# Kernel optimization log

Measured on AMD Instinct MI355X. Metric: run time of the kernel, lower is better.

The kernel has to match this reference:

```python
import jax, jax.numpy as jnp
import numpy as np

B, S, H = 2, 2048, 2048
NH, NKV, HD = 16, 4, 128
GROUPS = NH // NKV  # 4
ROPE_BASE = 10000.0


def _rope_tables(seq_len, dim):
    inv_freq = 1.0 / (ROPE_BASE ** (jnp.arange(0, dim, 2, dtype=jnp.float32) / dim))
    t = jnp.arange(seq_len, dtype=jnp.float32)
    freqs = jnp.outer(t, inv_freq)            # [S, HD/2]
    emb = jnp.concatenate([freqs, freqs], -1)  # [S, HD]
    return jnp.cos(emb), jnp.sin(emb)


def _rotate_half(x):
    x1, x2 = x[..., : x.shape[-1] // 2], x[..., x.shape[-1] // 2:]
    return jnp.concatenate([-x2, x1], axis=-1)


def setup_inputs() -> dict:
    key = jax.random.key(0)
    ks = jax.random.split(key, 5)
    hidden_states = jax.random.normal(ks[0], (B, S, H), dtype=jnp.float32)
    wq = jax.random.normal(ks[1], (H, NH * HD), dtype=jnp.float32) * 0.02
    wk = jax.random.normal(ks[2], (H, NKV * HD), dtype=jnp.float32) * 0.02
    wv = jax.random.normal(ks[3], (H, NKV * HD), dtype=jnp.float32) * 0.02
    wo = jax.random.normal(ks[4], (NH * HD, H), dtype=jnp.float32) * 0.02
    # additive causal mask [1,1,S,S]
    causal = jnp.tril(jnp.ones((S, S), dtype=bool))
    attention_mask = jnp.where(causal, 0.0, jnp.finfo(jnp.float32).min)[None, None]
    return {"hidden_states": hidden_states, "attention_mask": attention_mask,
            "wq": wq, "wk": wk, "wv": wv, "wo": wo}


def reference(hidden_states, attention_mask, wq, wk, wv, wo):
    b, s, _ = hidden_states.shape
    # projections -> [B, heads, S, HD]
    q = (hidden_states @ wq).reshape(b, s, NH, HD).transpose(0, 2, 1, 3)
    k = (hidden_states @ wk).reshape(b, s, NKV, HD).transpose(0, 2, 1, 3)
    v = (hidden_states @ wv).reshape(b, s, NKV, HD).transpose(0, 2, 1, 3)
    cos, sin = _rope_tables(s, HD)             # [S, HD]
    cos = cos[None, None]; sin = sin[None, None]
    q = q * cos + _rotate_half(q) * sin
    k = k * cos + _rotate_half(k) * sin
    # GQA: repeat kv heads (matches repeat_interleave on dim=1)
    k = jnp.repeat(k, GROUPS, axis=1)
    v = jnp.repeat(v, GROUPS, axis=1)
    scores = jnp.einsum("bhqd,bhkd->bhqk", q, k) / jnp.sqrt(jnp.float32(HD))
    scores = scores + attention_mask
    probs = jax.nn.softmax(scores.astype(jnp.float32), axis=-1).astype(q.dtype)
    attn = jnp.einsum("bhqk,bhkd->bhqd", probs, v)
    attn = attn.transpose(0, 2, 1, 3).reshape(b, s, NH * HD)
    return attn @ wo
```

## Files before the change

### kernel.cpp

```cpp
#include <hip/hip_runtime.h>

typedef unsigned short u16;
typedef unsigned int u32;
typedef __attribute__((ext_vector_type(8))) __bf16 bf16x8;
typedef __attribute__((ext_vector_type(8))) u16 u16x8;
typedef __attribute__((ext_vector_type(4))) float f32x4;

#define B_ 2
#define S_ 2048
#define H_ 2048
#define NH_ 16
#define NKV_ 4
#define HD_ 128
#define L2E 1.4426950408889634f

__device__ __forceinline__ u16 f2bf(float f) {
  return __builtin_bit_cast(u16, static_cast<__bf16>(f));
}
__device__ __forceinline__ float bf2f(u16 v) {
  return __builtin_bit_cast(float, (u32)v << 16);
}
__device__ __forceinline__ void gl2lds16(const void* g, void* l) {
  __builtin_amdgcn_global_load_lds((const __attribute__((address_space(1))) u32*)g,
                                   (__attribute__((address_space(3))) u32*)l, 16, 0, 0);
}
__device__ __forceinline__ f32x4 mfma16(bf16x8 a, bf16x8 b, f32x4 c) {
  return __builtin_amdgcn_mfma_f32_16x16x32_bf16(a, b, c, 0, 0, 0);
}

__global__ __launch_bounds__(256) void cvt_f32_bf16(const float* __restrict__ in,
                                                    u16* __restrict__ out) {
  size_t i = ((size_t)blockIdx.x * 256 + threadIdx.x) * 8;
  const float4* p = (const float4*)(in + i);
  float4 a = p[0], b = p[1];
  u16x8 o;
  o[0] = f2bf(a.x); o[1] = f2bf(a.y); o[2] = f2bf(a.z); o[3] = f2bf(a.w);
  o[4] = f2bf(b.x); o[5] = f2bf(b.y); o[6] = f2bf(b.z); o[7] = f2bf(b.w);
  *(u16x8*)(out + i) = o;
}

__global__ __launch_bounds__(256) void transpose_f32_bf16(const float* __restrict__ in,
                                                          u16* __restrict__ out,
                                                          int R, int C) {
  __shared__ float tl[32][33];
  int bx = blockIdx.x, by = blockIdx.y;
  int tx = threadIdx.x & 31, ty = threadIdx.x >> 5;
#pragma unroll
  for (int i = 0; i < 32; i += 8)
    tl[ty + i][tx] = in[(size_t)(by * 32 + ty + i) * C + bx * 32 + tx];
  __syncthreads();
#pragma unroll
  for (int i = 0; i < 32; i += 8)
    out[(size_t)(bx * 32 + ty + i) * R + by * 32 + tx] = f2bf(tl[tx][ty + i]);
}

__global__ __launch_bounds__(256) void transpose_v(const u16* __restrict__ kvb,
                                                   u16* __restrict__ vt) {
  __shared__ u16 tl[32][33];
  int sx = blockIdx.x, dx = blockIdx.y, b = blockIdx.z;
  int tx = threadIdx.x & 31, ty = threadIdx.x >> 5;
#pragma unroll
  for (int i = 0; i < 32; i += 8)
    tl[ty + i][tx] = kvb[(size_t)(b * S_ + sx * 32 + ty + i) * 1024 + 512 + dx * 32 + tx];
  __syncthreads();
#pragma unroll
  for (int i = 0; i < 32; i += 8)
    vt[(size_t)(b * 512 + dx * 32 + ty + i) * 2048 + sx * 32 + tx] = tl[tx][ty + i];
}

__global__ __launch_bounds__(256) void rope_kernel(u16* __restrict__ buf, int rstride,
                                                   int nhshift, float scale) {
  int idx = blockIdx.x * 256 + threadIdx.x;
  int grp = idx & 7;
  int h = (idx >> 3) & ((1 << nhshift) - 1);
  int tok = idx >> (3 + nhshift);
  int s = tok & (S_ - 1);
  u16* p = buf + (size_t)tok * rstride + (h << 7) + grp * 8;
  u16x8 lo = *(u16x8*)p;
  u16x8 hi = *(u16x8*)(p + 64);
  u16x8 olo, ohi;
#pragma unroll
  for (int j = 0; j < 8; j++) {
    int i = grp * 8 + j;
    float inv = exp2f((float)i * -0.20762050593045702f);
    float ang = (float)s * inv;
    float c = cosf(ang) * scale, sn = sinf(ang) * scale;
    float xl = bf2f(lo[j]), xh = bf2f(hi[j]);
    olo[j] = f2bf(xl * c - xh * sn);
    ohi[j] = f2bf(xh * c + xl * sn);
  }
  *(u16x8*)p = olo;
  *(u16x8*)(p + 64) = ohi;
}

template <int MODE>
__global__ __launch_bounds__(256) void gemm_bt(const u16* __restrict__ A,
                                               const u16* __restrict__ BT,
                                               void* __restrict__ C0,
                                               void* __restrict__ C1,
                                               int M, int N, int K) {
  __shared__ u16 As[2 * 128 * 32];
  __shared__ u16 Bs[2 * 128 * 32];
  const int Mt = M >> 7;
  const int nwg = gridDim.x;
  int wg = (blockIdx.x & 7) * (nwg >> 3) + (blockIdx.x >> 3);
  int tm = wg % Mt, tn = wg / Mt;
  const size_t m0 = (size_t)tm << 7, n0 = (size_t)tn << 7;
  const int tid = threadIdx.x;
  const int w = tid >> 6, lane = tid & 63;
  const int g = lane >> 4, l15 = lane & 15;
  const int wr = w >> 1, wc = w & 1;

  const int r0 = tid >> 2, s0 = tid & 3;
  const int r1 = (tid + 256) >> 2, s1 = (tid + 256) & 3;
  const u16* Ar0 = A + (m0 + r0) * K + s0 * 8;
  const u16* Ar1 = A + (m0 + r1) * K + s1 * 8;
  const u16* Br0 = BT + (n0 + r0) * K + s0 * 8;
  const u16* Br1 = BT + (n0 + r1) * K + s1 * 8;

  const f32x4 Z4 = {0.f, 0.f, 0.f, 0.f};
  f32x4 acc[4][4];
#pragma unroll
  for (int m = 0; m < 4; m++)
#pragma unroll
    for (int n = 0; n < 4; n++) acc[m][n] = Z4;

  gl2lds16(Ar0, &As[w * 512]);
  gl2lds16(Ar1, &As[w * 512 + 2048]);
  gl2lds16(Br0, &Bs[w * 512]);
  gl2lds16(Br1, &Bs[w * 512 + 2048]);

  const int nk = K >> 5;
  int cur = 0;
  for (int t = 0; t < nk; ++t) {
    if (t + 1 < nk) {
      const int k0 = (t + 1) << 5;
      const int nb = (cur ^ 1) << 12;
      gl2lds16(Ar0 + k0, &As[nb + w * 512]);
      gl2lds16(Ar1 + k0, &As[nb + w * 512 + 2048]);
      gl2lds16(Br0 + k0, &Bs[nb + w * 512]);
      gl2lds16(Br1 + k0, &Bs[nb + w * 512 + 2048]);
      asm volatile("s_waitcnt vmcnt(4)" ::: "memory");
    } else {
      asm volatile("s_waitcnt vmcnt(0)" ::: "memory");
    }
    __builtin_amdgcn_sched_barrier(0);
    __builtin_amdgcn_s_barrier();
    __builtin_amdgcn_sched_barrier(0);
    const int cb = cur << 12;
    bf16x8 af[4], bfr[4];
#pragma unroll
    for (int m = 0; m < 4; m++)
      af[m] = *(const bf16x8*)&As[cb + (wr * 64 + m * 16 + l15) * 32 + g * 8];
#pragma unroll
    for (int n = 0; n < 4; n++)
      bfr[n] = *(const bf16x8*)&Bs[cb + (wc * 64 + n * 16 + l15) * 32 + g * 8];
#pragma unroll
    for (int m = 0; m < 4; m++)
#pragma unroll
      for (int n = 0; n < 4; n++) acc[m][n] = mfma16(af[m], bfr[n], acc[m][n]);
    __builtin_amdgcn_sched_barrier(0);
    __builtin_amdgcn_s_barrier();
    __builtin_amdgcn_sched_barrier(0);
    cur ^= 1;
  }

  if (MODE == 2) {
    float* C = (float*)C0;
#pragma unroll
    for (int m = 0; m < 4; m++)
#pragma unroll
      for (int n = 0; n < 4; n++)
#pragma unroll
        for (int r = 0; r < 4; r++) {
          size_t row = m0 + wr * 64 + m * 16 + g * 4 + r;
          size_t col = n0 + wc * 64 + n * 16 + l15;
          C[row * (size_t)N + col] = acc[m][n][r];
        }
  } else {
    u16* C;
    size_t cs, cbase;
    if (n0 < 2048) { C = (u16*)C0; cs = 2048; cbase = n0; }
    else           { C = (u16*)C1; cs = 1024; cbase = n0 - 2048; }
#pragma unroll
    for (int m = 0; m < 4; m++)
#pragma unroll
      for (int n = 0; n < 4; n++)
#pragma unroll
        for (int r = 0; r < 4; r++) {
          size_t row = m0 + wr * 64 + m * 16 + g * 4 + r;
          C[row * cs + cbase + wc * 64 + n * 16 + l15] = f2bf(acc[m][n][r]);
        }
  }
}

__global__ __launch_bounds__(256) void attn_kernel(const u16* __restrict__ Qb,
                                                   const u16* __restrict__ KVb,
                                                   const u16* __restrict__ Vt,
                                                   u16* __restrict__ Ob) {
  __shared__ u16 Ks[2][64 * 128];
  __shared__ u16 Vs[2][128 * 64];
  __shared__ u16 Ps[4][16 * 72];
  const int pair = blockIdx.x, h = blockIdx.y, b = blockIdx.z;
  const int kvh = h >> 2;
  const int tid = threadIdx.x, w = tid >> 6, lane = tid & 63;
  const int g = lane >> 4, l15 = lane & 15;
  const f32x4 Z4 = {0.f, 0.f, 0.f, 0.f};
  u16x8 oneu;
#pragma unroll
  for (int j = 0; j < 8; j++) oneu[j] = 0x3f80;
  const bf16x8 ones = __builtin_bit_cast(bf16x8, oneu);

  const u16* Kbase = KVb + (size_t)b * S_ * 1024 + kvh * 128;
  const u16* Vbase = Vt + (size_t)(b * NKV_ + kvh) * HD_ * 2048;

  for (int half = 0; half < 2; ++half) {
    const int qt = half ? pair : 31 - pair;
    const int qrow0 = qt * 64 + w * 16;

    bf16x8 qf[4];
    const u16* qp = Qb + (size_t)(b * S_ + qrow0 + l15) * 2048 + h * 128;
#pragma unroll
    for (int ds = 0; ds < 4; ds++) qf[ds] = *(const bf16x8*)(qp + ds * 32 + g * 8);

    float m_r[4], l_r[4];
    f32x4 oa[8];
#pragma unroll
    for (int r = 0; r < 4; r++) { m_r[r] = -1e30f; l_r[r] = 0.f; }
#pragma unroll
    for (int n = 0; n < 8; n++) oa[n] = Z4;

    const int nt = qt + 1;
#pragma unroll
    for (int ro = 0; ro < 4; ++ro) {
      int c = ro * 256 + tid;
      int kv = c >> 4, p = c & 15;
      gl2lds16(Kbase + (size_t)kv * 1024 + 8 * (p ^ (kv & 15)), &Ks[0][ro * 2048 + w * 512]);
      int d = c >> 3, p2 = c & 7;
      gl2lds16(Vbase + (size_t)d * 2048 + 8 * (p2 ^ (d & 7)), &Vs[0][ro * 2048 + w * 512]);
    }
    __syncthreads();
    int cur = 0;

    for (int t = 0; t < nt; ++t) {
      const int kv0 = t * 64;
      if (t + 1 < nt) {
        const int nkv0 = kv0 + 64;
#pragma unroll
        for (int ro = 0; ro < 4; ++ro) {
          int c = ro * 256 + tid;
          int kv = c >> 4, p = c & 15;
          gl2lds16(Kbase + (size_t)(nkv0 + kv) * 1024 + 8 * (p ^ (kv & 15)),
                   &Ks[cur ^ 1][ro * 2048 + w * 512]);
          int d = c >> 3, p2 = c & 7;
          gl2lds16(Vbase + (size_t)d * 2048 + nkv0 + 8 * (p2 ^ (d & 7)),
                   &Vs[cur ^ 1][ro * 2048 + w * 512]);
        }
      }

      f32x4 sa[4];
#pragma unroll
      for (int c16 = 0; c16 < 4; c16++) sa[c16] = Z4;
      __builtin_amdgcn_s_setprio(1);
#pragma unroll
      for (int ds = 0; ds < 4; ++ds) {
#pragma unroll
        for (int c16 = 0; c16 < 4; ++c16) {
          bf16x8 kf = *(const bf16x8*)&Ks[cur][(c16 * 16 + l15) * 128 + ((ds * 4 + g) ^ l15) * 8];
          sa[c16] = mfma16(qf[ds], kf, sa[c16]);
        }
      }
      __builtin_amdgcn_s_setprio(0);

      if (kv0 + 63 > qrow0) {
#pragma unroll
        for (int c16 = 0; c16 < 4; c16++)
#pragma unroll
          for (int r = 0; r < 4; r++) {
            if (kv0 + c16 * 16 + l15 > qrow0 + g * 4 + r) sa[c16][r] = -1e30f;
          }
      }

      float lmax[4];
#pragma unroll
      for (int r = 0; r < 4; r++)
        lmax[r] = fmaxf(fmaxf(sa[0][r], sa[1][r]), fmaxf(sa[2][r], sa[3][r]));
      bool need = (lmax[0] > m_r[0] + 8.f) || (lmax[1] > m_r[1] + 8.f) ||
                  (lmax[2] > m_r[2] + 8.f) || (lmax[3] > m_r[3] + 8.f);
      if (__any(need)) {
        float pm[4];
#pragma unroll
        for (int r = 0; r < 4; r++) pm[r] = lmax[r];
#pragma unroll
        for (int off = 1; off < 16; off <<= 1)
#pragma unroll
          for (int r = 0; r < 4; r++) pm[r] = fmaxf(pm[r], __shfl_xor(pm[r], off));
#pragma unroll
        for (int r = 0; r < 4; r++) {
          float mn = fmaxf(m_r[r], pm[r]);
          float corr = exp2f((m_r[r] - mn) * L2E);
          m_r[r] = mn;
          l_r[r] *= corr;
#pragma unroll
          for (int n = 0; n < 8; n++) oa[n][r] *= corr;
        }
      }

#pragma unroll
      for (int c16 = 0; c16 < 4; c16++)
#pragma unroll
        for (int r = 0; r < 4; r++)
          Ps[w][(g * 4 + r) * 72 + c16 * 16 + l15] =
              f2bf(exp2f((sa[c16][r] - m_r[r]) * L2E));
      asm volatile("s_waitcnt lgkmcnt(0)" ::: "memory");
      __builtin_amdgcn_sched_barrier(0);

      f32x4 srow = Z4;
      __builtin_amdgcn_s_setprio(1);
#pragma unroll
      for (int ks = 0; ks < 2; ++ks) {
        bf16x8 pa = *(const bf16x8*)&Ps[w][l15 * 72 + ks * 32 + g * 8];
        srow = mfma16(pa, ones, srow);
#pragma unroll
        for (int n = 0; n < 8; n++) {
          bf16x8 vf = *(const bf16x8*)&Vs[cur][(n * 16 + l15) * 64 + (((ks * 4 + g) ^ (l15 & 7))) * 8];
          oa[n] = mfma16(pa, vf, oa[n]);
        }
      }
      __builtin_amdgcn_s_setprio(0);
#pragma unroll
      for (int r = 0; r < 4; r++) l_r[r] += srow[r];

      __syncthreads();
      cur ^= 1;
    }

    float inv[4];
#pragma unroll
    for (int r = 0; r < 4; r++) inv[r] = 1.0f / l_r[r];
#pragma unroll
    for (int n = 0; n < 8; n++)
#pragma unroll
      for (int r = 0; r < 4; r++) {
        size_t row = (size_t)b * S_ + qrow0 + g * 4 + r;
        Ob[row * 2048 + h * 128 + n * 16 + l15] = f2bf(oa[n][r] * inv[r]);
      }
  }
}

extern "C" void kernel_launch(void* const* d_in, const int* in_sizes, int n_in,
                              void* d_out, int out_size, void* d_ws, size_t ws_size,
                              hipStream_t stream) {
  const float* hid = (const float*)d_in[0];
  const float* wq = (const float*)d_in[2];
  const float* wk = (const float*)d_in[3];
  const float* wv = (const float*)d_in[4];
  const float* wo = (const float*)d_in[5];
  float* out = (float*)d_out;
  char* ws = (char*)d_ws;

  u16* hb     = (u16*)(ws);
  u16* wqkvT  = (u16*)(ws + (16u << 20));
  u16* Vt     = (u16*)(ws + (16u << 20));
  u16* woT    = (u16*)(ws + (20u << 20));
  u16* Qb     = (u16*)(ws + (28u << 20));
  u16* KVb    = (u16*)(ws + (44u << 20));

  cvt_f32_bf16<<<4096, 256, 0, stream>>>(hid, hb);
  transpose_f32_bf16<<<dim3(64, 64), 256, 0, stream>>>(wq, wqkvT, 2048, 2048);
  transpose_f32_bf16<<<dim3(16, 64), 256, 0, stream>>>(wk, wqkvT + (size_t)2048 * 2048, 2048, 512);
  transpose_f32_bf16<<<dim3(16, 64), 256, 0, stream>>>(wv, wqkvT + (size_t)2560 * 2048, 2048, 512);

  gemm_bt<1><<<768, 256, 0, stream>>>(hb, wqkvT, Qb, KVb, 4096, 3072, 2048);

  rope_kernel<<<2048, 256, 0, stream>>>(Qb, 2048, 4, 0.08838834764831845f);
  rope_kernel<<<512, 256, 0, stream>>>(KVb, 1024, 2, 1.0f);

  transpose_v<<<dim3(64, 16, 2), 256, 0, stream>>>(KVb, Vt);
  transpose_f32_bf16<<<dim3(64, 64), 256, 0, stream>>>(wo, woT, 2048, 2048);

  attn_kernel<<<dim3(16, 16, 2), 256, 0, stream>>>(Qb, KVb, Vt, hb);

  gemm_bt<2><<<512, 256, 0, stream>>>(hb, woT, out, nullptr, 4096, 2048, 2048);
}
```

Before: 238.6 us.

## Fuse RoPE into QKV GEMM epilogue via permuted B-row loading

Removes the two standalone RoPE kernels and applies rotary embedding and the Q scale inside the QKV projection GEMM epilogue. B-tile rows are loaded with a permutation so that each lane holds both the lo and hi halves of a head dimension pair in its accumulators. This saves a full read-modify-write pass over Q and K in bf16 plus two kernel launches. In exchange the epilogue now computes sin and cos per element and does scattered stores.

```diff
diff --git a/kernel.cpp b/kernel.cpp
--- a/kernel.cpp
+++ b/kernel.cpp
@@ -66,31 +66,6 @@
 #pragma unroll
   for (int i = 0; i < 32; i += 8)
     vt[(size_t)(b * 512 + dx * 32 + ty + i) * 2048 + sx * 32 + tx] = tl[tx][ty + i];
-}
-
-__global__ __launch_bounds__(256) void rope_kernel(u16* __restrict__ buf, int rstride,
-                                                   int nhshift, float scale) {
-  int idx = blockIdx.x * 256 + threadIdx.x;
-  int grp = idx & 7;
-  int h = (idx >> 3) & ((1 << nhshift) - 1);
-  int tok = idx >> (3 + nhshift);
-  int s = tok & (S_ - 1);
-  u16* p = buf + (size_t)tok * rstride + (h << 7) + grp * 8;
-  u16x8 lo = *(u16x8*)p;
-  u16x8 hi = *(u16x8*)(p + 64);
-  u16x8 olo, ohi;
-#pragma unroll
-  for (int j = 0; j < 8; j++) {
-    int i = grp * 8 + j;
-    float inv = exp2f((float)i * -0.20762050593045702f);
-    float ang = (float)s * inv;
-    float c = cosf(ang) * scale, sn = sinf(ang) * scale;
-    float xl = bf2f(lo[j]), xh = bf2f(hi[j]);
-    olo[j] = f2bf(xl * c - xh * sn);
-    ohi[j] = f2bf(xh * c + xl * sn);
-  }
-  *(u16x8*)p = olo;
-  *(u16x8*)(p + 64) = ohi;
 }
 
 template <int MODE>
@@ -111,12 +86,17 @@
   const int g = lane >> 4, l15 = lane & 15;
   const int wr = w >> 1, wc = w & 1;
 
+  const bool doRope = (MODE == 1) && (n0 < 2560);
+
   const int r0 = tid >> 2, s0 = tid & 3;
   const int r1 = (tid + 256) >> 2, s1 = (tid + 256) & 3;
+  auto sig = [&](int s) {
+    return doRope ? (((s >> 4) & 1) * 64 + (s >> 6) * 32 + ((s >> 5) & 1) * 16 + (s & 15)) : s;
+  };
   const u16* Ar0 = A + (m0 + r0) * K + s0 * 8;
   const u16* Ar1 = A + (m0 + r1) * K + s1 * 8;
-  const u16* Br0 = BT + (n0 + r0) * K + s0 * 8;
-  const u16* Br1 = BT + (n0 + r1) * K + s1 * 8;
+  const u16* Br0 = BT + (n0 + sig(r0)) * K + s0 * 8;
+  const u16* Br1 = BT + (n0 + sig(r1)) * K + s1 * 8;
 
   const f32x4 Z4 = {0.f, 0.f, 0.f, 0.f};
   f32x4 acc[4][4];
@@ -180,17 +160,39 @@
   } else {
     u16* C;
     size_t cs, cbase;
-    if (n0 < 2048) { C = (u16*)C0; cs = 2048; cbase = n0; }
-    else           { C = (u16*)C1; cs = 1024; cbase = n0 - 2048; }
-#pragma unroll
-    for (int m = 0; m < 4; m++)
-#pragma unroll
-      for (int n = 0; n < 4; n++)
-#pragma unroll
-        for (int r = 0; r < 4; r++) {
-          size_t row = m0 + wr * 64 + m * 16 + g * 4 + r;
-          C[row * cs + cbase + wc * 64 + n * 16 + l15] = f2bf(acc[m][n][r]);
-        }
+    float scale;
+    if (n0 < 2048) { C = (u16*)C0; cs = 2048; cbase = n0; scale = 0.08838834764831845f; }
+    else           { C = (u16*)C1; cs = 1024; cbase = n0 - 2048; scale = 1.0f; }
+    if (doRope) {
+#pragma unroll
+      for (int m = 0; m < 4; m++)
+#pragma unroll
+        for (int p = 0; p < 2; p++) {
+          const int d = wc * 32 + p * 16 + l15;
+          const float inv = exp2f((float)d * -0.20762050593045702f);
+          const float lo0 = acc[m][2 * p][0], hi0 = acc[m][2 * p + 1][0];
+          (void)lo0; (void)hi0;
+#pragma unroll
+          for (int r = 0; r < 4; r++) {
+            size_t row = m0 + wr * 64 + m * 16 + g * 4 + r;
+            float ang = (float)(int)(row & (S_ - 1)) * inv;
+            float c = cosf(ang) * scale, sn = sinf(ang) * scale;
+            float lo = acc[m][2 * p][r], hi = acc[m][2 * p + 1][r];
+            C[row * cs + cbase + d] = f2bf(lo * c - hi * sn);
+            C[row * cs + cbase + d + 64] = f2bf(hi * c + lo * sn);
+          }
+        }
+    } else {
+#pragma unroll
+      for (int m = 0; m < 4; m++)
+#pragma unroll
+        for (int n = 0; n < 4; n++)
+#pragma unroll
+          for (int r = 0; r < 4; r++) {
+            size_t row = m0 + wr * 64 + m * 16 + g * 4 + r;
+            C[row * cs + cbase + wc * 64 + n * 16 + l15] = f2bf(acc[m][n][r]);
+          }
+    }
   }
 }
 
@@ -373,9 +375,6 @@
 
   gemm_bt<1><<<768, 256, 0, stream>>>(hb, wqkvT, Qb, KVb, 4096, 3072, 2048);
 
-  rope_kernel<<<2048, 256, 0, stream>>>(Qb, 2048, 4, 0.08838834764831845f);
-  rope_kernel<<<512, 256, 0, stream>>>(KVb, 1024, 2, 1.0f);
-
   transpose_v<<<dim3(64, 16, 2), 256, 0, stream>>>(KVb, Vt);
   transpose_f32_bf16<<<dim3(64, 64), 256, 0, stream>>>(wo, woT, 2048, 2048);
 
```

After: 245.9 us. 1.03x slower.
